# Kernel tuning notes

Hardware: AMD Instinct MI355X
Metric: run time of the kernel (lower is better)

## Reference

```python
import jax, jax.numpy as jnp
import numpy as np

D = 1024
H = 16
HD = D // H
DFF = 4 * D
LN_EPS = 1e-5

def layernorm(x, gamma, beta):
    mu = jnp.mean(x, axis=-1, keepdims=True)
    var = jnp.mean(jnp.square(x - mu), axis=-1, keepdims=True)
    return (x - mu) * jax.lax.rsqrt(var + LN_EPS) * gamma + beta

def setup_inputs() -> dict:
    key = jax.random.key(0)
    ks = jax.random.split(key, 10)
    B, Nq, Nk = 2, 2048, 2048
    s = 0.02
    return {
        "q_x": jax.random.normal(ks[0], (B, Nq, D), jnp.float32),
        "kv_x": jax.random.normal(ks[1], (B, Nk, D), jnp.float32),
        "Wq": jax.random.normal(ks[2], (D, D), jnp.float32) * s,
        "Wkv": jax.random.normal(ks[3], (2 * D, D), jnp.float32) * s,
        "Wo": jax.random.normal(ks[4], (D, D), jnp.float32) * s,
        "bo": jnp.zeros((D,), jnp.float32),
        "ln_q_g": jnp.ones((D,), jnp.float32),
        "ln_q_b": jnp.zeros((D,), jnp.float32),
        "ln_kv_g": jnp.ones((D,), jnp.float32),
        "ln_kv_b": jnp.zeros((D,), jnp.float32),
        "W1": jax.random.normal(ks[5], (DFF, D), jnp.float32) * s,
        "b1": jnp.zeros((DFF,), jnp.float32),
        "W2": jax.random.normal(ks[6], (D, DFF), jnp.float32) * s,
        "b2": jnp.zeros((D,), jnp.float32),
    }

def reference(q_x, kv_x, Wq, Wkv, Wo, bo, ln_q_g, ln_q_b, ln_kv_g, ln_kv_b, W1, b1, W2, b2):
    B, Nq, _ = q_x.shape
    Nk = kv_x.shape[1]
    scale = HD ** -0.5
    # norm + projections
    q = layernorm(q_x, ln_q_g, ln_q_b) @ Wq.T                    # [B,Nq,D]
    kv = layernorm(kv_x, ln_kv_g, ln_kv_b) @ Wkv.T               # [B,Nk,2D]
    q = q.reshape(B, Nq, H, HD).transpose(0, 2, 1, 3)            # [B,H,Nq,hd]
    kv = kv.reshape(B, Nk, 2, H, HD).transpose(2, 0, 3, 1, 4)    # [2,B,H,Nk,hd]
    k, v = kv[0], kv[1]
    attn = jnp.einsum('bhqd,bhkd->bhqk', q, k) * scale           # [B,H,Nq,Nk]
    attn = jax.nn.softmax(attn, axis=-1)
    out = jnp.einsum('bhqk,bhkd->bhqd', attn, v)
    out = out.transpose(0, 2, 1, 3).reshape(B, Nq, D)
    x = q_x + out @ Wo.T + bo
    h = jax.nn.silu(x @ W1.T + b1)
    x = x + h @ W2.T + b2
    return x
```

## Files before the change

kernel.cpp:

```cpp
#include <hip/hip_runtime.h>

using u16   = unsigned short;
using f32x4 = __attribute__((ext_vector_type(4))) float;
using s16x8 = __attribute__((ext_vector_type(8))) short;
using u32x2 = __attribute__((ext_vector_type(2))) unsigned int;
using u32x4 = __attribute__((ext_vector_type(4))) unsigned int;

#define LOG2E 1.44269504088896f

static __device__ __forceinline__ u16 f2bf(float f) {
  union { float f; unsigned u; } a; a.f = f;
  unsigned r = a.u + 0x7fffu + ((a.u >> 16) & 1u);
  return (u16)(r >> 16);
}
static __device__ __forceinline__ unsigned cvtpk(float lo, float hi) {
  unsigned r;
  asm("v_cvt_pk_bf16_f32 %0, %1, %2" : "=v"(r) : "v"(lo), "v"(hi));
  return r;
}

static __device__ __forceinline__ void gload16(const void* g, void* l) {
  __builtin_amdgcn_global_load_lds(
      (__attribute__((address_space(1))) unsigned int*)g,
      (__attribute__((address_space(3))) unsigned int*)l, 16, 0, 0);
}

__global__ __launch_bounds__(256) void prep_k(
    const float* __restrict__ Wq, const float* __restrict__ Wkv,
    const float* __restrict__ Wo, const float* __restrict__ W1,
    const float* __restrict__ W2,
    u16* __restrict__ wq_b, u16* __restrict__ wkv_b, u16* __restrict__ wo_b,
    u16* __restrict__ w1_b, u16* __restrict__ w2_b,
    const float* __restrict__ xq, const float* __restrict__ xk,
    const float* __restrict__ gq, const float* __restrict__ bq,
    const float* __restrict__ gk, const float* __restrict__ bk,
    u16* __restrict__ oq, u16* __restrict__ ok)
{
  const int blk = blockIdx.x, t = threadIdx.x;
  if (blk < 12288) {
    const int i = blk * 256 + t;
    const float* src; u16* dst; int off; float sc = 1.0f;
    if      (i <  262144) { src = Wq;  dst = wq_b;  off = i; sc = 0.125f * LOG2E; }
    else if (i <  786432) { src = Wkv; dst = wkv_b; off = i -  262144; }
    else if (i < 1048576) { src = Wo;  dst = wo_b;  off = i -  786432; }
    else if (i < 2097152) { src = W1;  dst = w1_b;  off = i - 1048576; }
    else                  { src = W2;  dst = w2_b;  off = i - 2097152; }
    const float4 v = ((const float4*)src)[off];
    ushort4 o;
    o.x = f2bf(v.x * sc); o.y = f2bf(v.y * sc); o.z = f2bf(v.z * sc); o.w = f2bf(v.w * sc);
    ((ushort4*)dst)[off] = o;
    return;
  }
  int row = blk - 12288;
  const float* x; const float* gam; const float* bet; u16* out;
  if (row < 4096) { x = xq; gam = gq; bet = bq; out = oq; }
  else { row -= 4096; x = xk; gam = gk; bet = bk; out = ok; }
  const float4 v = ((const float4*)(x + (size_t)row * 1024))[t];
  float s  = v.x + v.y + v.z + v.w;
  float ss = v.x*v.x + v.y*v.y + v.z*v.z + v.w*v.w;
  #pragma unroll
  for (int m = 1; m < 64; m <<= 1) { s += __shfl_xor(s, m); ss += __shfl_xor(ss, m); }
  __shared__ float red[8];
  const int w = t >> 6;
  if ((t & 63) == 0) { red[w] = s; red[4 + w] = ss; }
  __syncthreads();
  s  = red[0] + red[1] + red[2] + red[3];
  ss = red[4] + red[5] + red[6] + red[7];
  const float mu   = s * (1.0f / 1024.0f);
  const float rstd = rsqrtf(ss * (1.0f / 1024.0f) - mu * mu + 1e-5f);
  const float4 gv = ((const float4*)gam)[t];
  const float4 bv = ((const float4*)bet)[t];
  ushort4 o;
  o.x = f2bf((v.x - mu) * rstd * gv.x + bv.x);
  o.y = f2bf((v.y - mu) * rstd * gv.y + bv.y);
  o.z = f2bf((v.z - mu) * rstd * gv.z + bv.z);
  o.w = f2bf((v.w - mu) * rstd * gv.w + bv.w);
  ((ushort4*)(out + (size_t)row * 1024))[t] = o;
}

template<int BIAS, int RES, int SILU, int OF32, int OBF>
static __device__ __forceinline__ void gemm_body(
    const u16* __restrict__ A, const u16* __restrict__ B,
    u16* __restrict__ Cb, float* __restrict__ Cf,
    const float* __restrict__ bias, const float* __restrict__ resid,
    int N, int K, int bid, u16* smem)
{
  const int tid = threadIdx.x;
  const int w = tid >> 6, l = tid & 63;
  const int g = l >> 4, q = l & 15;
  const int ntn = N >> 7;
  const int bm = bid / ntn, bn = bid - bm * ntn;
  const int wr = w >> 1, wc = w & 1;
  const int sw = (q & 7) << 4;
  f32x4 acc[2][4] = {};

  const size_t abase = (size_t)(bm * 128) * K;
  const size_t bbase = (size_t)(bn * 128) * K;

  auto stage = [&](int buf, int k0) {
    u16* as = smem + buf * 8192;
    u16* bs = smem + 16384 + buf * 8192;
    #pragma unroll
    for (int r = 0; r < 2; ++r) {
      const int c = (r << 9) + tid;
      const int row = c >> 3, part = c & 7;
      const int sp = part ^ (row & 7);
      gload16(A + abase + (size_t)row * K + k0 + sp * 8,
              as + (size_t)((r << 9) + (w << 6)) * 8);
      gload16(B + bbase + (size_t)row * K + k0 + sp * 8,
              bs + (size_t)((r << 9) + (w << 6)) * 8);
    }
  };

  const int NT = K >> 6;
  stage(0, 0);
  asm volatile("s_waitcnt vmcnt(0)" ::: "memory");
  __syncthreads();
  int cur = 0;
  for (int t = 0; t < NT; ++t) {
    if (t + 1 < NT) stage(cur ^ 1, (t + 1) << 6);
    const char* as = (const char*)(smem + cur * 8192);
    const char* bs = (const char*)(smem + 16384 + cur * 8192);
    #pragma unroll
    for (int ks = 0; ks < 2; ++ks) {
      s16x8 af[2], bfr[4];
      #pragma unroll
      for (int m = 0; m < 2; ++m)
        af[m] = *(const s16x8*)(as + (size_t)(wr * 32 + m * 16 + q) * 128 +
                                ((ks * 64 + g * 16) ^ sw));
      #pragma unroll
      for (int n = 0; n < 4; ++n)
        bfr[n] = *(const s16x8*)(bs + (size_t)(wc * 64 + n * 16 + q) * 128 +
                                 ((ks * 64 + g * 16) ^ sw));
      #pragma unroll
      for (int m = 0; m < 2; ++m)
        #pragma unroll
        for (int n = 0; n < 4; ++n)
          acc[m][n] = __builtin_amdgcn_mfma_f32_16x16x32_bf16(af[m], bfr[n], acc[m][n], 0, 0, 0);
    }
    asm volatile("s_waitcnt vmcnt(0)" ::: "memory");
    __syncthreads();
    cur ^= 1;
  }

  #pragma unroll
  for (int m = 0; m < 2; ++m) {
    const int row0 = bm * 128 + wr * 32 + m * 16 + g * 4;
    #pragma unroll
    for (int n = 0; n < 4; ++n) {
      const int col = bn * 128 + wc * 64 + n * 16 + q;
      float bv = 0.0f;
      if (BIAS) bv = bias[col];
      #pragma unroll
      for (int r = 0; r < 4; ++r) {
        const size_t idx = (size_t)(row0 + r) * N + col;
        float v = acc[m][n][r] + bv;
        if (RES)  v += resid[idx];
        if (SILU) v = v / (1.0f + __expf(-v));
        if (OF32) Cf[idx] = v;
        if (OBF)  Cb[idx] = f2bf(v);
      }
    }
  }
}

template<int BIAS, int RES, int SILU, int OF32, int OBF>
__global__ __launch_bounds__(512, 4) void gemm_k(
    const u16* __restrict__ A, const u16* __restrict__ B,
    u16* __restrict__ Cb, float* __restrict__ Cf,
    const float* __restrict__ bias, const float* __restrict__ resid,
    int N, int K)
{
  __shared__ u16 smem[32768];
  gemm_body<BIAS, RES, SILU, OF32, OBF>(A, B, Cb, Cf, bias, resid, N, K, blockIdx.x, smem);
}

__global__ __launch_bounds__(512, 4) void gemm_qkv_k(
    const u16* __restrict__ lnq, const u16* __restrict__ wq, u16* __restrict__ qp,
    const u16* __restrict__ lnk, const u16* __restrict__ wkv, u16* __restrict__ kvp)
{
  __shared__ u16 smem[32768];
  if (blockIdx.x < 256)
    gemm_body<0,0,0,0,1>(lnq, wq, qp, nullptr, nullptr, nullptr, 1024, 1024, blockIdx.x, smem);
  else
    gemm_body<0,0,0,0,1>(lnk, wkv, kvp, nullptr, nullptr, nullptr, 2048, 1024, blockIdx.x - 256, smem);
}

__global__ __launch_bounds__(256, 4) void attn_k(
    const u16* __restrict__ Q, const u16* __restrict__ KV, u16* __restrict__ O)
{
  __shared__ u16 Ks[2][64 * 64];
  __shared__ u16 Vs[2][64 * 64];
  const int tid = threadIdx.x;
  const int w = tid >> 6, l = tid & 63;
  const int g = l >> 4, q = l & 15;
  const int bh = blockIdx.x >> 5, qt = blockIdx.x & 31;
  const int b = bh >> 4, h = bh & 15;

  const size_t qrow = (size_t)(b * 2048 + qt * 64 + w * 16 + q);
  s16x8 qf[2];
  qf[0] = *(const s16x8*)&Q[qrow * 1024 + h * 64 + g * 8];
  qf[1] = *(const s16x8*)&Q[qrow * 1024 + h * 64 + 32 + g * 8];

  f32x4 oacc[4] = {};
  float mrow = -1e30f, lrow = 0.0f;

  const u16* kvb = KV + (size_t)b * 2048 * 2048;
  const unsigned vs_base =
      (unsigned)(unsigned long long)(__attribute__((address_space(3))) u16*)Vs;

  auto stage = [&](int buf, int kv0) {
    #pragma unroll
    for (int r = 0; r < 2; ++r) {
      const int c = (r << 8) + tid;
      const int krow = c >> 3, slot = c & 7;
      gload16(kvb + (size_t)(kv0 + krow) * 2048 + h * 64 + ((slot ^ (krow & 7)) << 3),
              &Ks[buf][(size_t)((r << 8) + (w << 6)) * 8]);
      const int vkv = ((c >> 3) & 15) * 4 + ((c >> 1) & 3);
      const int vd0 = ((c >> 7) & 3) * 16 + (c & 1) * 8;
      gload16(kvb + (size_t)(kv0 + vkv) * 2048 + 1024 + h * 64 + vd0,
              &Vs[buf][(size_t)((r << 8) + (w << 6)) * 8]);
    }
  };

  stage(0, 0);
  asm volatile("s_waitcnt vmcnt(0)" ::: "memory");
  __syncthreads();
  int cur = 0;

  for (int kt = 0; kt < 32; ++kt) {
    if (kt + 1 < 32) stage(cur ^ 1, (kt + 1) * 64);

    const char* ksb = (const char*)Ks[cur];
    f32x4 sacc[4] = {};
    __builtin_amdgcn_s_setprio(1);
    #pragma unroll
    for (int s = 0; s < 2; ++s)
      #pragma unroll
      for (int nf = 0; nf < 4; ++nf) {
        const int krw = nf * 16 + q;
        const s16x8 kf = *(const s16x8*)(ksb + krw * 128 +
                              ((s * 64 + g * 16) ^ ((krw & 7) << 4)));
        sacc[nf] = __builtin_amdgcn_mfma_f32_16x16x32_bf16(kf, qf[s], sacc[nf], 0, 0, 0);
      }
    __builtin_amdgcn_s_setprio(0);

    float mx = sacc[0][0];
    #pragma unroll
    for (int nf = 0; nf < 4; ++nf)
      #pragma unroll
      for (int r = 0; r < 4; ++r) mx = fmaxf(mx, sacc[nf][r]);
    mx = fmaxf(mx, __shfl_xor(mx, 16));
    mx = fmaxf(mx, __shfl_xor(mx, 32));
    if (__any(mx > mrow + 8.0f)) {
      const float mnew = fmaxf(mrow, mx);
      const float al = __builtin_amdgcn_exp2f(mrow - mnew);
      lrow *= al;
      float ar[4];
      #pragma unroll
      for (int r = 0; r < 4; ++r) ar[r] = __shfl(al, g * 4 + r);
      #pragma unroll
      for (int nf = 0; nf < 4; ++nf)
        #pragma unroll
        for (int r = 0; r < 4; ++r) oacc[nf][r] *= ar[r];
      mrow = mnew;
    }
    float rs = 0.0f;
    #pragma unroll
    for (int nf = 0; nf < 4; ++nf)
      #pragma unroll
      for (int r = 0; r < 4; ++r) {
        const float e = __builtin_amdgcn_exp2f(sacc[nf][r] - mrow);
        sacc[nf][r] = e; rs += e;
      }
    rs += __shfl_xor(rs, 16);
    rs += __shfl_xor(rs, 32);
    lrow += rs;

    const unsigned vsb = vs_base + (unsigned)(cur << 13);
    __builtin_amdgcn_s_setprio(1);
    #pragma unroll
    for (int s = 0; s < 2; ++s) {
      union { u32x4 u; s16x8 s8; } au;
      au.u[0] = cvtpk(sacc[2*s  ][0], sacc[2*s  ][1]);
      au.u[1] = cvtpk(sacc[2*s  ][2], sacc[2*s  ][3]);
      au.u[2] = cvtpk(sacc[2*s+1][0], sacc[2*s+1][1]);
      au.u[3] = cvtpk(sacc[2*s+1][2], sacc[2*s+1][3]);
      #pragma unroll
      for (int nf = 0; nf < 4; ++nf) {
        const unsigned a1 = vsb + (unsigned)((nf * 16 + 8 * s + g) * 128 + 2 * q);
        u32x2 t1, t2;
        asm volatile("ds_read_b64_tr_b16 %0, %2\n\t"
                     "ds_read_b64_tr_b16 %1, %2 offset:512\n\t"
                     "s_waitcnt lgkmcnt(0)"
                     : "=&v"(t1), "=&v"(t2) : "v"(a1) : "memory");
        __builtin_amdgcn_sched_barrier(0);
        union { u32x4 u; s16x8 s8; } bu;
        bu.u[0] = t1[0]; bu.u[1] = t1[1]; bu.u[2] = t2[0]; bu.u[3] = t2[1];
        oacc[nf] = __builtin_amdgcn_mfma_f32_16x16x32_bf16(au.s8, bu.s8, oacc[nf], 0, 0, 0);
      }
    }
    __builtin_amdgcn_s_setprio(0);

    asm volatile("s_waitcnt vmcnt(0)" ::: "memory");
    __syncthreads();
    cur ^= 1;
  }

  float lr[4];
  #pragma unroll
  for (int r = 0; r < 4; ++r) lr[r] = __shfl(lrow, g * 4 + r);
  const size_t ob = (size_t)(b * 2048 + qt * 64 + w * 16) * 1024 + h * 64;
  #pragma unroll
  for (int r = 0; r < 4; ++r) {
    const float inv = 1.0f / lr[r];
    #pragma unroll
    for (int nf = 0; nf < 4; ++nf)
      O[ob + (size_t)(g * 4 + r) * 1024 + nf * 16 + q] = f2bf(oacc[nf][r] * inv);
  }
}

extern "C" void kernel_launch(void* const* d_in, const int* in_sizes, int n_in,
                              void* d_out, int out_size, void* d_ws, size_t ws_size,
                              hipStream_t stream)
{
  const float* q_x  = (const float*)d_in[0];
  const float* kv_x = (const float*)d_in[1];
  const float* Wq   = (const float*)d_in[2];
  const float* Wkv  = (const float*)d_in[3];
  const float* Wo   = (const float*)d_in[4];
  const float* bo   = (const float*)d_in[5];
  const float* lnqg = (const float*)d_in[6];
  const float* lnqb = (const float*)d_in[7];
  const float* lnkg = (const float*)d_in[8];
  const float* lnkb = (const float*)d_in[9];
  const float* W1   = (const float*)d_in[10];
  const float* b1   = (const float*)d_in[11];
  const float* W2   = (const float*)d_in[12];
  const float* b2   = (const float*)d_in[13];
  float* out = (float*)d_out;

  char* ws = (char*)d_ws;
  const size_t MB = 1024 * 1024;
  u16*   wq_b  = (u16*)  (ws +  0 * MB);
  u16*   wkv_b = (u16*)  (ws +  2 * MB);
  u16*   wo_b  = (u16*)  (ws +  6 * MB);
  u16*   w1_b  = (u16*)  (ws +  8 * MB);
  u16*   w2_b  = (u16*)  (ws + 16 * MB);
  u16*   lnq   = (u16*)  (ws + 24 * MB);
  u16*   lnk   = (u16*)  (ws + 32 * MB);
  u16*   qp    = (u16*)  (ws + 40 * MB);
  u16*   kvp   = (u16*)  (ws + 48 * MB);
  u16*   ao    = (u16*)  (ws + 64 * MB);
  float* xf    = (float*)(ws + 72 * MB);
  u16*   xb    = (u16*)  (ws + 88 * MB);
  u16*   hb    = (u16*)  (ws + 96 * MB);

  prep_k<<<dim3(20480), dim3(256), 0, stream>>>(
      Wq, Wkv, Wo, W1, W2, wq_b, wkv_b, wo_b, w1_b, w2_b,
      q_x, kv_x, lnqg, lnqb, lnkg, lnkb, lnq, lnk);

  gemm_qkv_k<<<dim3(768), dim3(512), 0, stream>>>(lnq, wq_b, qp, lnk, wkv_b, kvp);
  attn_k<<<dim3(1024), dim3(256), 0, stream>>>(qp, kvp, ao);
  gemm_k<1,1,0,1,1><<<dim3(256),  dim3(512), 0, stream>>>(
      ao, wo_b, xb, xf, bo, q_x, 1024, 1024);
  gemm_k<1,0,1,0,1><<<dim3(1024), dim3(512), 0, stream>>>(
      xb, w1_b, hb, nullptr, b1, nullptr, 4096, 1024);
  gemm_k<1,1,0,1,0><<<dim3(256),  dim3(512), 0, stream>>>(
      hb, w2_b, nullptr, out, b2, xf, 1024, 4096);
}
```

Before: 226.8 us.

## Use 256x256-tile GEMM for FFN up-projection and batch V transposed reads in attention

Adds a new GEMM kernel with 256x256 output tiles, a 128KB double-buffered LDS stage and an XCD-aware block remap. It is used for the W1+SiLU projection, launched with 256 blocks instead of 1024. Larger tiles raise operand reuse per LDS load, at the cost of more registers and LDS per block and fewer blocks to fill the CUs. Separately, the attention PV step now issues all 16 transposed V reads before a single wait instead of waiting after each pair, which hides LDS latency but raises register pressure.

```diff
diff --git a/kernel.cpp b/kernel.cpp
--- a/kernel.cpp
+++ b/kernel.cpp
@@ -186,6 +186,108 @@
     gemm_body<0,0,0,0,1>(lnk, wkv, kvp, nullptr, nullptr, nullptr, 2048, 1024, blockIdx.x - 256, smem);
 }
 
+template<int BIAS, int RES, int SILU, int OF32, int OBF>
+__global__ __launch_bounds__(512, 2) void gemm256_k(
+    const u16* __restrict__ A, const u16* __restrict__ B,
+    u16* __restrict__ Cb, float* __restrict__ Cf,
+    const float* __restrict__ bias, const float* __restrict__ resid,
+    int N, int K)
+{
+  __shared__ u16 smem[65536];
+  char* smem_c = (char*)smem;
+  const int tid = threadIdx.x;
+  const int w = tid >> 6, l = tid & 63;
+  const int g = l >> 4, q = l & 15;
+  const int wm = w >> 2, wn = w & 3;
+  const int ntn = N >> 8;
+  const int nwg = gridDim.x;
+  const int bid = (blockIdx.x % 8) * (nwg / 8) + blockIdx.x / 8;
+  const int bm = bid / ntn, bn = bid - bm * ntn;
+
+  const size_t abase = (size_t)(bm * 256) * K;
+  const size_t bbase = (size_t)(bn * 256) * K;
+
+  f32x4 acc[8][4] = {};
+
+  auto stage4 = [&](int buf, int kt, int halfsel) {
+    #pragma unroll
+    for (int rr = 0; rr < 4; ++rr) {
+      const int r = halfsel * 4 + rr;
+      const int isB   = (r >> 1) & 1;
+      const int khalf = r >> 2;
+      const int sub   = r & 1;
+      const int row   = sub * 128 + (tid >> 2);
+      const int slot  = (tid & 3) ^ ((row >> 1) & 3);
+      const u16* src = (isB ? B + bbase : A + abase)
+                     + (size_t)row * K + kt * 64 + khalf * 32 + slot * 8;
+      char* dst = smem_c + buf * 65536 + isB * 32768 + khalf * 16384
+                + sub * 8192 + w * 1024;
+      gload16(src, dst);
+    }
+  };
+
+  const int NT = K >> 6;
+  stage4(0, 0, 0); stage4(0, 0, 1);
+  int cur = 0;
+  for (int kt = 0; kt < NT; ++kt) {
+    const bool pre = (kt + 1 < NT);
+    if (pre) stage4(cur ^ 1, kt + 1, 0);
+    if (pre) asm volatile("s_waitcnt vmcnt(4)" ::: "memory");
+    else     asm volatile("s_waitcnt vmcnt(0)" ::: "memory");
+    __builtin_amdgcn_s_barrier();
+    asm volatile("" ::: "memory");
+    const char* Ab0 = smem_c + cur * 65536;
+    const char* Bb0 = Ab0 + 32768;
+    const int so = (g ^ ((q >> 1) & 3)) * 16;
+    #pragma unroll
+    for (int ks = 0; ks < 2; ++ks) {
+      const char* Ab = Ab0 + ks * 16384;
+      const char* Bb = Bb0 + ks * 16384;
+      s16x8 af[8], bfr[4];
+      #pragma unroll
+      for (int m = 0; m < 8; ++m)
+        af[m] = *(const s16x8*)(Ab + (wm * 128 + m * 16 + q) * 64 + so);
+      #pragma unroll
+      for (int n = 0; n < 4; ++n)
+        bfr[n] = *(const s16x8*)(Bb + (wn * 64 + n * 16 + q) * 64 + so);
+      if (ks == 0 && pre) stage4(cur ^ 1, kt + 1, 1);
+      asm volatile("s_waitcnt lgkmcnt(0)" ::: "memory");
+      __builtin_amdgcn_sched_barrier(0);
+      __builtin_amdgcn_s_setprio(1);
+      #pragma unroll
+      for (int m = 0; m < 8; ++m)
+        #pragma unroll
+        for (int n = 0; n < 4; ++n)
+          acc[m][n] = __builtin_amdgcn_mfma_f32_16x16x32_bf16(af[m], bfr[n], acc[m][n], 0, 0, 0);
+      __builtin_amdgcn_s_setprio(0);
+    }
+    asm volatile("" ::: "memory");
+    __builtin_amdgcn_s_barrier();
+    asm volatile("" ::: "memory");
+    cur ^= 1;
+  }
+
+  #pragma unroll
+  for (int m = 0; m < 8; ++m) {
+    const int row0 = bm * 256 + wm * 128 + m * 16 + g * 4;
+    #pragma unroll
+    for (int n = 0; n < 4; ++n) {
+      const int col = bn * 256 + wn * 64 + n * 16 + q;
+      float bv = 0.0f;
+      if (BIAS) bv = bias[col];
+      #pragma unroll
+      for (int r = 0; r < 4; ++r) {
+        const size_t idx = (size_t)(row0 + r) * N + col;
+        float v = acc[m][n][r] + bv;
+        if (RES)  v += resid[idx];
+        if (SILU) v = v / (1.0f + __expf(-v));
+        if (OF32) Cf[idx] = v;
+        if (OBF)  Cb[idx] = f2bf(v);
+      }
+    }
+  }
+}
+
 __global__ __launch_bounds__(256, 4) void attn_k(
     const u16* __restrict__ Q, const u16* __restrict__ KV, u16* __restrict__ O)
 {
@@ -277,28 +379,61 @@
     rs += __shfl_xor(rs, 32);
     lrow += rs;
 
-    const unsigned vsb = vs_base + (unsigned)(cur << 13);
+    union { u32x4 u; s16x8 s8; } au[2];
+    #pragma unroll
+    for (int s = 0; s < 2; ++s) {
+      au[s].u[0] = cvtpk(sacc[2*s  ][0], sacc[2*s  ][1]);
+      au[s].u[1] = cvtpk(sacc[2*s  ][2], sacc[2*s  ][3]);
+      au[s].u[2] = cvtpk(sacc[2*s+1][0], sacc[2*s+1][1]);
+      au[s].u[3] = cvtpk(sacc[2*s+1][2], sacc[2*s+1][3]);
+    }
+
+    const unsigned a0 = vs_base + (unsigned)(cur << 13) + (unsigned)(g * 128 + 2 * q);
+    u32x2 v0,v1,v2,v3,v4,v5,v6,v7,v8,v9,v10,v11,v12,v13,v14,v15;
+    asm volatile(
+        "ds_read_b64_tr_b16 %0,  %16\n\t"
+        "ds_read_b64_tr_b16 %1,  %16 offset:512\n\t"
+        "ds_read_b64_tr_b16 %2,  %16 offset:2048\n\t"
+        "ds_read_b64_tr_b16 %3,  %16 offset:2560\n\t"
+        "ds_read_b64_tr_b16 %4,  %16 offset:4096\n\t"
+        "ds_read_b64_tr_b16 %5,  %16 offset:4608\n\t"
+        "ds_read_b64_tr_b16 %6,  %16 offset:6144\n\t"
+        "ds_read_b64_tr_b16 %7,  %16 offset:6656\n\t"
+        "ds_read_b64_tr_b16 %8,  %16 offset:1024\n\t"
+        "ds_read_b64_tr_b16 %9,  %16 offset:1536\n\t"
+        "ds_read_b64_tr_b16 %10, %16 offset:3072\n\t"
+        "ds_read_b64_tr_b16 %11, %16 offset:3584\n\t"
+        "ds_read_b64_tr_b16 %12, %16 offset:5120\n\t"
+        "ds_read_b64_tr_b16 %13, %16 offset:5632\n\t"
+        "ds_read_b64_tr_b16 %14, %16 offset:7168\n\t"
+        "ds_read_b64_tr_b16 %15, %16 offset:7680\n\t"
+        "s_waitcnt lgkmcnt(0)"
+        : "=&v"(v0), "=&v"(v1), "=&v"(v2),  "=&v"(v3),
+          "=&v"(v4), "=&v"(v5), "=&v"(v6),  "=&v"(v7),
+          "=&v"(v8), "=&v"(v9), "=&v"(v10), "=&v"(v11),
+          "=&v"(v12),"=&v"(v13),"=&v"(v14), "=&v"(v15)
+        : "v"(a0) : "memory");
+    __builtin_amdgcn_sched_barrier(0);
+
     __builtin_amdgcn_s_setprio(1);
-    #pragma unroll
-    for (int s = 0; s < 2; ++s) {
-      union { u32x4 u; s16x8 s8; } au;
-      au.u[0] = cvtpk(sacc[2*s  ][0], sacc[2*s  ][1]);
-      au.u[1] = cvtpk(sacc[2*s  ][2], sacc[2*s  ][3]);
-      au.u[2] = cvtpk(sacc[2*s+1][0], sacc[2*s+1][1]);
-      au.u[3] = cvtpk(sacc[2*s+1][2], sacc[2*s+1][3]);
-      #pragma unroll
-      for (int nf = 0; nf < 4; ++nf) {
-        const unsigned a1 = vsb + (unsigned)((nf * 16 + 8 * s + g) * 128 + 2 * q);
-        u32x2 t1, t2;
-        asm volatile("ds_read_b64_tr_b16 %0, %2\n\t"
-                     "ds_read_b64_tr_b16 %1, %2 offset:512\n\t"
-                     "s_waitcnt lgkmcnt(0)"
-                     : "=&v"(t1), "=&v"(t2) : "v"(a1) : "memory");
-        __builtin_amdgcn_sched_barrier(0);
-        union { u32x4 u; s16x8 s8; } bu;
-        bu.u[0] = t1[0]; bu.u[1] = t1[1]; bu.u[2] = t2[0]; bu.u[3] = t2[1];
-        oacc[nf] = __builtin_amdgcn_mfma_f32_16x16x32_bf16(au.s8, bu.s8, oacc[nf], 0, 0, 0);
-      }
+    {
+      union { u32x4 u; s16x8 s8; } bu;
+      bu.u[0]=v0[0];  bu.u[1]=v0[1];  bu.u[2]=v1[0];  bu.u[3]=v1[1];
+      oacc[0] = __builtin_amdgcn_mfma_f32_16x16x32_bf16(au[0].s8, bu.s8, oacc[0], 0, 0, 0);
+      bu.u[0]=v2[0];  bu.u[1]=v2[1];  bu.u[2]=v3[0];  bu.u[3]=v3[1];
+      oacc[1] = __builtin_amdgcn_mfma_f32_16x16x32_bf16(au[0].s8, bu.s8, oacc[1], 0, 0, 0);
+      bu.u[0]=v4[0];  bu.u[1]=v4[1];  bu.u[2]=v5[0];  bu.u[3]=v5[1];
+      oacc[2] = __builtin_amdgcn_mfma_f32_16x16x32_bf16(au[0].s8, bu.s8, oacc[2], 0, 0, 0);
+      bu.u[0]=v6[0];  bu.u[1]=v6[1];  bu.u[2]=v7[0];  bu.u[3]=v7[1];
+      oacc[3] = __builtin_amdgcn_mfma_f32_16x16x32_bf16(au[0].s8, bu.s8, oacc[3], 0, 0, 0);
+      bu.u[0]=v8[0];  bu.u[1]=v8[1];  bu.u[2]=v9[0];  bu.u[3]=v9[1];
+      oacc[0] = __builtin_amdgcn_mfma_f32_16x16x32_bf16(au[1].s8, bu.s8, oacc[0], 0, 0, 0);
+      bu.u[0]=v10[0]; bu.u[1]=v10[1]; bu.u[2]=v11[0]; bu.u[3]=v11[1];
+      oacc[1] = __builtin_amdgcn_mfma_f32_16x16x32_bf16(au[1].s8, bu.s8, oacc[1], 0, 0, 0);
+      bu.u[0]=v12[0]; bu.u[1]=v12[1]; bu.u[2]=v13[0]; bu.u[3]=v13[1];
+      oacc[2] = __builtin_amdgcn_mfma_f32_16x16x32_bf16(au[1].s8, bu.s8, oacc[2], 0, 0, 0);
+      bu.u[0]=v14[0]; bu.u[1]=v14[1]; bu.u[2]=v15[0]; bu.u[3]=v15[1];
+      oacc[3] = __builtin_amdgcn_mfma_f32_16x16x32_bf16(au[1].s8, bu.s8, oacc[3], 0, 0, 0);
     }
     __builtin_amdgcn_s_setprio(0);
 
@@ -364,7 +499,7 @@
   attn_k<<<dim3(1024), dim3(256), 0, stream>>>(qp, kvp, ao);
   gemm_k<1,1,0,1,1><<<dim3(256),  dim3(512), 0, stream>>>(
       ao, wo_b, xb, xf, bo, q_x, 1024, 1024);
-  gemm_k<1,0,1,0,1><<<dim3(1024), dim3(512), 0, stream>>>(
+  gemm256_k<1,0,1,0,1><<<dim3(256), dim3(512), 0, stream>>>(
       xb, w1_b, hb, nullptr, b1, nullptr, 4096, 1024);
   gemm_k<1,1,0,1,0><<<dim3(256),  dim3(512), 0, stream>>>(
       hb, w2_b, nullptr, out, b2, xf, 1024, 4096);
```

Measured after the change: 227.4 us. No clear change (+0.3%).
